# Kernel optimization log

Measured on AMD Instinct MI355X. Metric: run time of the kernel, lower is better.

Reference implementation:

```python
import jax, jax.numpy as jnp
import numpy as np

B, C_IN, C_MID, C_OUT, R, K = 2048, 64, 64, 128, 60, 13
EPS = 1e-5


def _gather(x, nei):
    # x: [B, C, 60] -> gather neighbors -> [B, C, 60, 13]
    b, c = x.shape[0], x.shape[1]
    return x[:, :, nei].reshape(b, c, R, K)


def _block(x, nei, g, bta, m, v, W, c):
    # BN (eval mode) -> ReLU -> Conv2d(kernel (1,13)) fused block.
    h = _gather(x, nei)                              # [B,C,60,13]
    inv = g * jax.lax.rsqrt(v + EPS)                 # [C]
    h = jax.nn.relu(h * inv[None, :, None, None] + (bta - m * inv)[None, :, None, None])
    # Conv2d with kernel (1,13), stride 1 == contraction over (c, k)
    return jnp.einsum('bcrk,ock->bor', h, W) + c[None, :, None]  # [B,O,60]


def setup_inputs() -> dict:
    key = jax.random.key(0)
    ks = jax.random.split(key, 24)
    n = lambda k, s: jax.random.normal(k, s, dtype=jnp.float32)
    u = lambda k, s: jax.random.uniform(k, s, dtype=jnp.float32, minval=0.5, maxval=1.5)
    return {
        "x": n(ks[0], (B, C_IN, R)),
        "nei": jax.random.randint(ks[1], (R * K,), 0, R, dtype=jnp.int32),
        # comb_layer_in: BN(in) + Conv(in->mid)
        "g1": n(ks[2], (C_IN,)), "b1": n(ks[3], (C_IN,)), "m1": n(ks[4], (C_IN,)), "v1": u(ks[5], (C_IN,)),
        "W1": n(ks[6], (C_MID, C_IN, K)) * 0.1, "c1": n(ks[7], (C_MID,)) * 0.1,
        # comb_layer_out: BN(mid) + Conv(mid->out)
        "g2": n(ks[8], (C_MID,)), "b2": n(ks[9], (C_MID,)), "m2": n(ks[10], (C_MID,)), "v2": u(ks[11], (C_MID,)),
        "W2": n(ks[12], (C_OUT, C_MID, K)) * 0.1, "c2": n(ks[13], (C_OUT,)) * 0.1,
        # short_cut_layer: BN(in) + Conv(in->out)
        "g3": n(ks[14], (C_IN,)), "b3": n(ks[15], (C_IN,)), "m3": n(ks[16], (C_IN,)), "v3": u(ks[17], (C_IN,)),
        "W3": n(ks[18], (C_OUT, C_IN, K)) * 0.1, "c3": n(ks[19], (C_OUT,)) * 0.1,
    }


def reference(x, nei, g1, b1, m1, v1, W1, c1, g2, b2, m2, v2, W2, c2,
              g3, b3, m3, v3, W3, c3):
    f = _block(x, nei, g1, b1, m1, v1, W1, c1)      # [B, C_MID, 60]
    f = _block(f, nei, g2, b2, m2, v2, W2, c2)      # [B, C_OUT, 60]
    sc = _block(x, nei, g3, b3, m3, v3, W3, c3)     # [B, C_OUT, 60]
    return f + sc
```

## Files before the change

### kernel.cpp

```cpp
#include <hip/hip_runtime.h>
#include <hip/hip_bf16.h>


typedef __attribute__((ext_vector_type(8))) short bf16x8;
typedef __attribute__((ext_vector_type(4))) float f32x4;
typedef __attribute__((ext_vector_type(4))) unsigned short us4;
typedef __attribute__((ext_vector_type(8))) unsigned short us8;

#define EPSV 1e-5f
#define PLANE 131072
#define ZTOT  7864320

__device__ __forceinline__ unsigned short f2bf(float f) {
  unsigned int u = __builtin_bit_cast(unsigned int, f);
  u += 0x7FFFu + ((u >> 16) & 1u);
  return (unsigned short)(u >> 16);
}
__device__ __forceinline__ float bf2f(unsigned short s) {
  unsigned int u = ((unsigned int)s) << 16;
  return __builtin_bit_cast(float, u);
}

__global__ void prep_w(const float* __restrict__ W1, const float* __restrict__ W2,
                       const float* __restrict__ W3,
                       const float* __restrict__ g1, const float* __restrict__ be1,
                       const float* __restrict__ mu1, const float* __restrict__ va1,
                       const float* __restrict__ c1,
                       const float* __restrict__ g2, const float* __restrict__ be2,
                       const float* __restrict__ mu2, const float* __restrict__ va2,
                       const float* __restrict__ c2,
                       const float* __restrict__ g3, const float* __restrict__ be3,
                       const float* __restrict__ mu3, const float* __restrict__ va3,
                       const float* __restrict__ c3,
                       unsigned short* __restrict__ W1t,
                       unsigned short* __restrict__ W23t,
                       float* __restrict__ params) {
  int t = blockIdx.x * 256 + threadIdx.x;
  if (t < 4096) {
    int o = t >> 6, c = t & 63;
    const float* src = W1 + (o * 64 + c) * 13;
    unsigned short* dst = W1t + o * 832 + c;
    #pragma unroll
    for (int ks = 0; ks < 13; ks++) dst[ks * 64] = f2bf(src[ks]);
  } else if (t < 20480) {
    int idx = t - 4096;
    int half = idx >> 13;
    int o = (idx >> 6) & 127, c = idx & 63;
    const float* src = (half ? W3 : W2) + (o * 64 + c) * 13;
    unsigned short* dst = W23t + o * 1664 + half * 13 * 64 + c;
    #pragma unroll
    for (int ks = 0; ks < 13; ks++) dst[ks * 64] = f2bf(src[ks]);
  }
  if (blockIdx.x == 79) {
    int u = threadIdx.x;
    if (u < 64) {
      float a1v = g1[u] * rsqrtf(va1[u] + EPSV);
      params[u]       = a1v;
      params[64 + u]  = be1[u] - mu1[u] * a1v;
      float a3v = g3[u] * rsqrtf(va3[u] + EPSV);
      params[128 + u] = a3v;
      params[192 + u] = be3[u] - mu3[u] * a3v;
      float a2v = g2[u] * rsqrtf(va2[u] + EPSV);
      params[256 + u] = a2v;
      params[320 + u] = be2[u] - mu2[u] * a2v + a2v * c1[u];
    }
    if (u < 128) params[384 + u] = c2[u] + c3[u];
  }
}

__global__ __launch_bounds__(256) void t_in(const float* __restrict__ x,
                                            const float* __restrict__ params,
                                            unsigned short* __restrict__ z1T,
                                            unsigned short* __restrict__ z3T) {
  __shared__ float xt[64 * 61];
  __shared__ float prm[256];
  const int b = blockIdx.x, t = threadIdx.x;
  prm[t] = params[t];
  for (int i = t; i < 3840; i += 256) {
    int c = i / 60;
    xt[c * 61 + (i - c * 60)] = x[b * 3840 + i];
  }
  __syncthreads();
  if (t < 240) {
    int r = t >> 2, g = t & 3, c0 = g << 4;
    us8 z1v0, z1v1, z3v0, z3v1;
    #pragma unroll
    for (int j = 0; j < 8; j++) {
      int c = c0 + j;
      float v = xt[c * 61 + r];
      z1v0[j] = f2bf(fmaxf(fmaf(v, prm[c], prm[64 + c]), 0.f));
      z3v0[j] = f2bf(fmaxf(fmaf(v, prm[128 + c], prm[192 + c]), 0.f));
    }
    #pragma unroll
    for (int j = 0; j < 8; j++) {
      int c = c0 + 8 + j;
      float v = xt[c * 61 + r];
      z1v1[j] = f2bf(fmaxf(fmaf(v, prm[c], prm[64 + c]), 0.f));
      z3v1[j] = f2bf(fmaxf(fmaf(v, prm[128 + c], prm[192 + c]), 0.f));
    }
    int idx = (r * 2048 + b) * 64 + c0;
    *(us8*)(z1T + idx) = z1v0;  *(us8*)(z1T + idx + 8) = z1v1;
    *(us8*)(z3T + idx) = z3v0;  *(us8*)(z3T + idx + 8) = z3v1;
  }
}

#define MFMA __builtin_amdgcn_mfma_f32_16x16x32_bf16

__global__ __launch_bounds__(256, 2) void gemm1(const unsigned short* __restrict__ W1t,
                                                const unsigned short* __restrict__ z1T,
                                                const int* __restrict__ nei,
                                                const float* __restrict__ params,
                                                unsigned short* __restrict__ z2T) {
  __shared__ unsigned short As[2][4096];
  __shared__ unsigned short Bs[2][2][8192];

  const int bid = blockIdx.x;
  const int rp = bid >> 4, btile = bid & 15;
  const int b0 = btile << 7;
  const int rA = rp * 2, rB = rA + 1;
  const int t = threadIdx.x, wave = t >> 6, lane = t & 63;
  const int quad = lane >> 4, nl = lane & 15;
  const int rsel = wave >> 1, nhh = wave & 1;

  int pl0[13], pl1[13];
  #pragma unroll
  for (int q = 0; q < 13; q++) { pl0[q] = nei[rA * 13 + q]; pl1[q] = nei[rB * 13 + q]; }

  const int trow = t >> 3, tj = t & 7;
  const int sw8 = ((tj ^ (trow & 7)) << 3);
  const unsigned short* gA = W1t + trow * 832 + tj * 8;
  const unsigned short* gB = z1T + (b0 + trow) * 64 + tj * 8;
  unsigned short* lA = &As[0][trow * 64 + sw8];
  unsigned short* lB0 = &Bs[0][0][trow * 64 + sw8];
  unsigned short* lB1 = &Bs[0][1][trow * 64 + sw8];

  {
    us8 va0 = *(const us8*)(gA);
    us8 va1 = *(const us8*)(gA + 32 * 832);
    const unsigned short* g0 = gB + pl0[0] * PLANE;
    const unsigned short* g1p = gB + pl1[0] * PLANE;
    us8 b00 = *(const us8*)(g0);
    us8 b01 = *(const us8*)(g0 + 2048);
    us8 b02 = *(const us8*)(g0 + 4096);
    us8 b03 = *(const us8*)(g0 + 6144);
    us8 b10 = *(const us8*)(g1p);
    us8 b11 = *(const us8*)(g1p + 2048);
    us8 b12 = *(const us8*)(g1p + 4096);
    us8 b13 = *(const us8*)(g1p + 6144);
    *(us8*)(lA) = va0;  *(us8*)(lA + 2048) = va1;
    *(us8*)(lB0) = b00; *(us8*)(lB0 + 2048) = b01;
    *(us8*)(lB0 + 4096) = b02; *(us8*)(lB0 + 6144) = b03;
    *(us8*)(lB1) = b10; *(us8*)(lB1 + 2048) = b11;
    *(us8*)(lB1 + 4096) = b12; *(us8*)(lB1 + 6144) = b13;
  }
  __syncthreads();

  const int c0 = ((quad ^ (nl & 7)) << 3);
  f32x4 acc[4][4] = {};
  #pragma unroll 1
  for (int kq = 0; kq < 13; kq++) {
    const int bf = kq & 1;
    us8 va0, va1, b00, b01, b02, b03, b10, b11, b12, b13;
    if (kq < 12) {
      const unsigned short* ga = gA + (kq + 1) * 64;
      va0 = *(const us8*)(ga);
      va1 = *(const us8*)(ga + 32 * 832);
      const unsigned short* g0 = gB + pl0[kq + 1] * PLANE;
      const unsigned short* g1p = gB + pl1[kq + 1] * PLANE;
      b00 = *(const us8*)(g0);        b01 = *(const us8*)(g0 + 2048);
      b02 = *(const us8*)(g0 + 4096); b03 = *(const us8*)(g0 + 6144);
      b10 = *(const us8*)(g1p);        b11 = *(const us8*)(g1p + 2048);
      b12 = *(const us8*)(g1p + 4096); b13 = *(const us8*)(g1p + 6144);
    }
    const unsigned short* Ab = &As[bf][nl * 64];
    const unsigned short* Bb = &Bs[bf][rsel][(nhh * 64 + nl) * 64];
    bf16x8 af[4][2], bfr[4][2];
    #pragma unroll
    for (int mt = 0; mt < 4; mt++) {
      af[mt][0] = *(const bf16x8*)(Ab + mt * 1024 + c0);
      af[mt][1] = *(const bf16x8*)(Ab + mt * 1024 + (c0 ^ 32));
    }
    #pragma unroll
    for (int nt = 0; nt < 4; nt++) {
      bfr[nt][0] = *(const bf16x8*)(Bb + nt * 1024 + c0);
      bfr[nt][1] = *(const bf16x8*)(Bb + nt * 1024 + (c0 ^ 32));
    }
    #pragma unroll
    for (int h = 0; h < 2; h++)
      #pragma unroll
      for (int mt = 0; mt < 4; mt++)
        #pragma unroll
        for (int nt = 0; nt < 4; nt++)
          acc[mt][nt] = MFMA(af[mt][h], bfr[nt][h], acc[mt][nt], 0, 0, 0);
    if (kq < 12) {
      unsigned short* la = lA + (bf ^ 1) * 4096;
      unsigned short* l0 = lB0 + (bf ^ 1) * 16384;
      unsigned short* l1 = lB1 + (bf ^ 1) * 16384;
      *(us8*)(la) = va0;  *(us8*)(la + 2048) = va1;
      *(us8*)(l0) = b00; *(us8*)(l0 + 2048) = b01;
      *(us8*)(l0 + 4096) = b02; *(us8*)(l0 + 6144) = b03;
      *(us8*)(l1) = b10; *(us8*)(l1 + 2048) = b11;
      *(us8*)(l1 + 4096) = b12; *(us8*)(l1 + 6144) = b13;
    }
    __syncthreads();
  }

  const int rr = rA + rsel;
  #pragma unroll
  for (int mt = 0; mt < 4; mt++) {
    int ob = mt * 16 + quad * 4;
    f32x4 av = *(const f32x4*)(params + 256 + ob);
    f32x4 bv = *(const f32x4*)(params + 320 + ob);
    #pragma unroll
    for (int nt = 0; nt < 4; nt++) {
      int col = b0 + nhh * 64 + nt * 16 + nl;
      f32x4 a = acc[mt][nt];
      us4 w;
      w.x = f2bf(fmaxf(fmaf(a[0], av[0], bv[0]), 0.f));
      w.y = f2bf(fmaxf(fmaf(a[1], av[1], bv[1]), 0.f));
      w.z = f2bf(fmaxf(fmaf(a[2], av[2], bv[2]), 0.f));
      w.w = f2bf(fmaxf(fmaf(a[3], av[3], bv[3]), 0.f));
      *(us4*)(z2T + (rr * 2048 + col) * 64 + ob) = w;
    }
  }
}

__global__ __launch_bounds__(256, 2) void gemm2(const unsigned short* __restrict__ W23t,
                                                const unsigned short* __restrict__ z2T,
                                                const unsigned short* __restrict__ z3T,
                                                const int* __restrict__ nei,
                                                const float* __restrict__ params,
                                                unsigned short* __restrict__ outT) {
  __shared__ unsigned short As[2][8192];
  __shared__ unsigned short Bs[2][8192];

  const int bid = blockIdx.x;
  const int r = bid >> 4, btile = bid & 15;
  const int b0 = btile << 7;
  const int t = threadIdx.x, wave = t >> 6, lane = t & 63;
  const int quad = lane >> 4, nl = lane & 15;
  const int mh = wave >> 1, nh = wave & 1;

  int pl[13];
  #pragma unroll
  for (int q = 0; q < 13; q++) pl[q] = nei[r * 13 + q];

  const int trow = t >> 3, tj = t & 7;
  const int sw8 = ((tj ^ (trow & 7)) << 3);
  const unsigned short* gA  = W23t + trow * 1664 + tj * 8;
  const unsigned short* gB2 = z2T + (b0 + trow) * 64 + tj * 8;
  const unsigned short* gB3 = z3T + (b0 + trow) * 64 + tj * 8;
  unsigned short* lA = &As[0][trow * 64 + sw8];
  unsigned short* lB = &Bs[0][trow * 64 + sw8];

  {
    us8 va0 = *(const us8*)(gA);
    us8 va1 = *(const us8*)(gA + 32 * 1664);
    us8 va2 = *(const us8*)(gA + 64 * 1664);
    us8 va3 = *(const us8*)(gA + 96 * 1664);
    const unsigned short* gb = gB2 + pl[0] * PLANE;
    us8 vb0 = *(const us8*)(gb);
    us8 vb1 = *(const us8*)(gb + 2048);
    us8 vb2 = *(const us8*)(gb + 4096);
    us8 vb3 = *(const us8*)(gb + 6144);
    *(us8*)(lA) = va0;        *(us8*)(lA + 2048) = va1;
    *(us8*)(lA + 4096) = va2; *(us8*)(lA + 6144) = va3;
    *(us8*)(lB) = vb0;        *(us8*)(lB + 2048) = vb1;
    *(us8*)(lB + 4096) = vb2; *(us8*)(lB + 6144) = vb3;
  }
  __syncthreads();

  const int c0 = ((quad ^ (nl & 7)) << 3);
  f32x4 acc[4][4] = {};
  #pragma unroll 1
  for (int kq = 0; kq < 26; kq++) {
    const int bf = kq & 1;
    us8 va0, va1, va2, va3, vb0, vb1, vb2, vb3;
    if (kq < 25) {
      const int kn = kq + 1;
      const unsigned short* ga = gA + kn * 64;
      va0 = *(const us8*)(ga);
      va1 = *(const us8*)(ga + 32 * 1664);
      va2 = *(const us8*)(ga + 64 * 1664);
      va3 = *(const us8*)(ga + 96 * 1664);
      const unsigned short* gb = (kn < 13) ? (gB2 + pl[kn] * PLANE)
                                           : (gB3 + pl[kn - 13] * PLANE);
      vb0 = *(const us8*)(gb);
      vb1 = *(const us8*)(gb + 2048);
      vb2 = *(const us8*)(gb + 4096);
      vb3 = *(const us8*)(gb + 6144);
    }
    const unsigned short* Ab = &As[bf][(mh * 64 + nl) * 64];
    const unsigned short* Bb = &Bs[bf][(nh * 64 + nl) * 64];
    bf16x8 af[4][2], bfr[4][2];
    #pragma unroll
    for (int mt = 0; mt < 4; mt++) {
      af[mt][0] = *(const bf16x8*)(Ab + mt * 1024 + c0);
      af[mt][1] = *(const bf16x8*)(Ab + mt * 1024 + (c0 ^ 32));
    }
    #pragma unroll
    for (int nt = 0; nt < 4; nt++) {
      bfr[nt][0] = *(const bf16x8*)(Bb + nt * 1024 + c0);
      bfr[nt][1] = *(const bf16x8*)(Bb + nt * 1024 + (c0 ^ 32));
    }
    #pragma unroll
    for (int h = 0; h < 2; h++)
      #pragma unroll
      for (int mt = 0; mt < 4; mt++)
        #pragma unroll
        for (int nt = 0; nt < 4; nt++)
          acc[mt][nt] = MFMA(af[mt][h], bfr[nt][h], acc[mt][nt], 0, 0, 0);
    if (kq < 25) {
      unsigned short* la = lA + (bf ^ 1) * 8192;
      unsigned short* lb = lB + (bf ^ 1) * 8192;
      *(us8*)(la) = va0;        *(us8*)(la + 2048) = va1;
      *(us8*)(la + 4096) = va2; *(us8*)(la + 6144) = va3;
      *(us8*)(lb) = vb0;        *(us8*)(lb + 2048) = vb1;
      *(us8*)(lb + 4096) = vb2; *(us8*)(lb + 6144) = vb3;
    }
    __syncthreads();
  }

  #pragma unroll
  for (int mt = 0; mt < 4; mt++) {
    int ob = mh * 64 + mt * 16 + quad * 4;
    f32x4 cv = *(const f32x4*)(params + 384 + ob);
    #pragma unroll
    for (int nt = 0; nt < 4; nt++) {
      int col = b0 + nh * 64 + nt * 16 + nl;
      f32x4 a = acc[mt][nt];
      us4 w;
      w.x = f2bf(a[0] + cv[0]);
      w.y = f2bf(a[1] + cv[1]);
      w.z = f2bf(a[2] + cv[2]);
      w.w = f2bf(a[3] + cv[3]);
      *(us4*)(outT + (r * 2048 + col) * 128 + ob) = w;
    }
  }
}

__global__ __launch_bounds__(256) void t_out(const unsigned short* __restrict__ outT,
                                             float* __restrict__ out) {
  __shared__ float ot[60 * 129];
  const int b = blockIdx.x, t = threadIdx.x;
  for (int i = t; i < 1920; i += 256) {
    int r = i >> 5, og = (i & 31) << 2;
    us4 v = *(const us4*)(outT + (r * 2048 + b) * 128 + og);
    ot[r * 129 + og + 0] = bf2f(v.x);
    ot[r * 129 + og + 1] = bf2f(v.y);
    ot[r * 129 + og + 2] = bf2f(v.z);
    ot[r * 129 + og + 3] = bf2f(v.w);
  }
  __syncthreads();
  int o = t >> 1, s = t & 1;
  float* dst = out + b * 7680 + o * 60 + s * 30;
  #pragma unroll
  for (int j = 0; j < 30; j++) dst[j] = ot[(s * 30 + j) * 129 + o];
}

extern "C" void kernel_launch(void* const* d_in, const int* in_sizes, int n_in,
                              void* d_out, int out_size, void* d_ws, size_t ws_size,
                              hipStream_t stream) {
  const float* x   = (const float*)d_in[0];
  const int*   nei = (const int*)d_in[1];
  const float* g1  = (const float*)d_in[2];
  const float* be1 = (const float*)d_in[3];
  const float* mu1 = (const float*)d_in[4];
  const float* va1 = (const float*)d_in[5];
  const float* W1  = (const float*)d_in[6];
  const float* c1  = (const float*)d_in[7];
  const float* g2  = (const float*)d_in[8];
  const float* be2 = (const float*)d_in[9];
  const float* mu2 = (const float*)d_in[10];
  const float* va2 = (const float*)d_in[11];
  const float* W2  = (const float*)d_in[12];
  const float* c2  = (const float*)d_in[13];
  const float* g3  = (const float*)d_in[14];
  const float* be3 = (const float*)d_in[15];
  const float* mu3 = (const float*)d_in[16];
  const float* va3 = (const float*)d_in[17];
  const float* W3  = (const float*)d_in[18];
  const float* c3  = (const float*)d_in[19];

  unsigned short* W1t  = (unsigned short*)d_ws;
  unsigned short* W23t = W1t + 53248;
  float*          prm  = (float*)(W23t + 212992);
  unsigned short* z2T  = (unsigned short*)(prm + 512);
  unsigned short* z3T  = z2T + ZTOT;
  unsigned short* big  = z3T + ZTOT;
  unsigned short* z1T  = big;
  unsigned short* outT = big;

  prep_w<<<80, 256, 0, stream>>>(W1, W2, W3,
                                 g1, be1, mu1, va1, c1,
                                 g2, be2, mu2, va2, c2,
                                 g3, be3, mu3, va3, c3,
                                 W1t, W23t, prm);
  t_in<<<2048, 256, 0, stream>>>(x, prm, z1T, z3T);
  gemm1<<<480, 256, 0, stream>>>(W1t, z1T, nei, prm, z2T);
  gemm2<<<960, 256, 0, stream>>>(W23t, z2T, z3T, nei, prm, outT);
  t_out<<<2048, 256, 0, stream>>>(outT, (float*)d_out);
}
```

Measured before the change: 245.3 us.

## Drop LDS staging in gemm2; load MFMA fragments directly from global

gemm2 no longer stages A and B tiles through double-buffered shared memory with barriers. Each wave now loads its MFMA fragments straight from global memory (relying on L1/L2 for reuse), and launch bounds rise from 2 to 4 blocks per CU. This removes LDS traffic and __syncthreads, and with the smaller register and LDS footprint more waves can hide latency. In exchange, each fragment is fetched by several waves, so global/L2 traffic grows and the explicit software prefetch pipeline is gone.

```diff
diff --git a/kernel.cpp b/kernel.cpp
--- a/kernel.cpp
+++ b/kernel.cpp
@@ -225,15 +225,12 @@
   }
 }
 
-__global__ __launch_bounds__(256, 2) void gemm2(const unsigned short* __restrict__ W23t,
+__global__ __launch_bounds__(256, 4) void gemm2(const unsigned short* __restrict__ W23t,
                                                 const unsigned short* __restrict__ z2T,
                                                 const unsigned short* __restrict__ z3T,
                                                 const int* __restrict__ nei,
                                                 const float* __restrict__ params,
                                                 unsigned short* __restrict__ outT) {
-  __shared__ unsigned short As[2][8192];
-  __shared__ unsigned short Bs[2][8192];
-
   const int bid = blockIdx.x;
   const int r = bid >> 4, btile = bid & 15;
   const int b0 = btile << 7;
@@ -245,80 +242,30 @@
   #pragma unroll
   for (int q = 0; q < 13; q++) pl[q] = nei[r * 13 + q];
 
-  const int trow = t >> 3, tj = t & 7;
-  const int sw8 = ((tj ^ (trow & 7)) << 3);
-  const unsigned short* gA  = W23t + trow * 1664 + tj * 8;
-  const unsigned short* gB2 = z2T + (b0 + trow) * 64 + tj * 8;
-  const unsigned short* gB3 = z3T + (b0 + trow) * 64 + tj * 8;
-  unsigned short* lA = &As[0][trow * 64 + sw8];
-  unsigned short* lB = &Bs[0][trow * 64 + sw8];
-
-  {
-    us8 va0 = *(const us8*)(gA);
-    us8 va1 = *(const us8*)(gA + 32 * 1664);
-    us8 va2 = *(const us8*)(gA + 64 * 1664);
-    us8 va3 = *(const us8*)(gA + 96 * 1664);
-    const unsigned short* gb = gB2 + pl[0] * PLANE;
-    us8 vb0 = *(const us8*)(gb);
-    us8 vb1 = *(const us8*)(gb + 2048);
-    us8 vb2 = *(const us8*)(gb + 4096);
-    us8 vb3 = *(const us8*)(gb + 6144);
-    *(us8*)(lA) = va0;        *(us8*)(lA + 2048) = va1;
-    *(us8*)(lA + 4096) = va2; *(us8*)(lA + 6144) = va3;
-    *(us8*)(lB) = vb0;        *(us8*)(lB + 2048) = vb1;
-    *(us8*)(lB + 4096) = vb2; *(us8*)(lB + 6144) = vb3;
-  }
-  __syncthreads();
-
-  const int c0 = ((quad ^ (nl & 7)) << 3);
+  const unsigned short* Abase = W23t + (mh * 64 + nl) * 1664 + quad * 8;
+  const int Boff = (b0 + nh * 64 + nl) * 64 + quad * 8;
+
   f32x4 acc[4][4] = {};
   #pragma unroll 1
   for (int kq = 0; kq < 26; kq++) {
-    const int bf = kq & 1;
-    us8 va0, va1, va2, va3, vb0, vb1, vb2, vb3;
-    if (kq < 25) {
-      const int kn = kq + 1;
-      const unsigned short* ga = gA + kn * 64;
-      va0 = *(const us8*)(ga);
-      va1 = *(const us8*)(ga + 32 * 1664);
-      va2 = *(const us8*)(ga + 64 * 1664);
-      va3 = *(const us8*)(ga + 96 * 1664);
-      const unsigned short* gb = (kn < 13) ? (gB2 + pl[kn] * PLANE)
-                                           : (gB3 + pl[kn - 13] * PLANE);
-      vb0 = *(const us8*)(gb);
-      vb1 = *(const us8*)(gb + 2048);
-      vb2 = *(const us8*)(gb + 4096);
-      vb3 = *(const us8*)(gb + 6144);
-    }
-    const unsigned short* Ab = &As[bf][(mh * 64 + nl) * 64];
-    const unsigned short* Bb = &Bs[bf][(nh * 64 + nl) * 64];
-    bf16x8 af[4][2], bfr[4][2];
-    #pragma unroll
-    for (int mt = 0; mt < 4; mt++) {
-      af[mt][0] = *(const bf16x8*)(Ab + mt * 1024 + c0);
-      af[mt][1] = *(const bf16x8*)(Ab + mt * 1024 + (c0 ^ 32));
-    }
-    #pragma unroll
-    for (int nt = 0; nt < 4; nt++) {
-      bfr[nt][0] = *(const bf16x8*)(Bb + nt * 1024 + c0);
-      bfr[nt][1] = *(const bf16x8*)(Bb + nt * 1024 + (c0 ^ 32));
-    }
-    #pragma unroll
-    for (int h = 0; h < 2; h++)
+    const unsigned short* Ak = Abase + kq * 64;
+    const unsigned short* Bk = (kq < 13 ? z2T + pl[kq] * PLANE
+                                        : z3T + pl[kq - 13] * PLANE) + Boff;
+    #pragma unroll
+    for (int h = 0; h < 2; h++) {
+      bf16x8 af[4], bfr[4];
+      #pragma unroll
+      for (int mt = 0; mt < 4; mt++)
+        af[mt] = *(const bf16x8*)(Ak + mt * 26624 + h * 32);
+      #pragma unroll
+      for (int nt = 0; nt < 4; nt++)
+        bfr[nt] = *(const bf16x8*)(Bk + nt * 1024 + h * 32);
       #pragma unroll
       for (int mt = 0; mt < 4; mt++)
         #pragma unroll
         for (int nt = 0; nt < 4; nt++)
-          acc[mt][nt] = MFMA(af[mt][h], bfr[nt][h], acc[mt][nt], 0, 0, 0);
-    if (kq < 25) {
-      unsigned short* la = lA + (bf ^ 1) * 8192;
-      unsigned short* lb = lB + (bf ^ 1) * 8192;
-      *(us8*)(la) = va0;        *(us8*)(la + 2048) = va1;
-      *(us8*)(la + 4096) = va2; *(us8*)(la + 6144) = va3;
-      *(us8*)(lb) = vb0;        *(us8*)(lb + 2048) = vb1;
-      *(us8*)(lb + 4096) = vb2; *(us8*)(lb + 6144) = vb3;
-    }
-    __syncthreads();
+          acc[mt][nt] = MFMA(af[mt], bfr[nt], acc[mt][nt], 0, 0, 0);
+    }
   }
 
   #pragma unroll
```

After: 372.9 us. 1.52x slower.
